# Performance work log

Hardware: AMD Instinct MI355X
Metric: run time of the kernel (lower is better)

The kernel has to match this reference:

```python
import jax, jax.numpy as jnp
import numpy as np

B, T, I = 16384, 101, 4
H = 512  # lstm_hidden_layer_size
M = 512  # mlp_hidden_layer_size


def setup_inputs() -> dict:
    key = jax.random.key(0)
    ks = jax.random.split(key, 10)
    s_ih = 1.0 / np.sqrt(H)
    inp = {
        "batch_x": jax.random.normal(ks[0], (B, T, I), dtype=jnp.float32),
        "batch_a": jax.random.uniform(ks[1], (B, 1), dtype=jnp.float32),
        # PyTorch nn.LSTM params (gate order i,f,g,o), U(-1/sqrt(H), 1/sqrt(H))
        "W_ih": jax.random.uniform(ks[2], (4 * H, I), minval=-s_ih, maxval=s_ih, dtype=jnp.float32),
        "W_hh": jax.random.uniform(ks[3], (4 * H, H), minval=-s_ih, maxval=s_ih, dtype=jnp.float32),
        "b_ih": jax.random.uniform(ks[4], (4 * H,), minval=-s_ih, maxval=s_ih, dtype=jnp.float32),
        "b_hh": jax.random.uniform(ks[5], (4 * H,), minval=-s_ih, maxval=s_ih, dtype=jnp.float32),
        "W1": jax.random.uniform(ks[6], (M, H), minval=-s_ih, maxval=s_ih, dtype=jnp.float32),
        "b1": jax.random.uniform(ks[7], (M,), minval=-s_ih, maxval=s_ih, dtype=jnp.float32),
        "W2": jax.random.uniform(ks[8], (1, M + 1), minval=-1.0 / np.sqrt(M + 1), maxval=1.0 / np.sqrt(M + 1), dtype=jnp.float32),
        "b2": jax.random.uniform(ks[9], (1,), minval=-1.0 / np.sqrt(M + 1), maxval=1.0 / np.sqrt(M + 1), dtype=jnp.float32),
    }
    return inp


def _lstm_last_hidden(batch_x, W_ih, W_hh, b_ih, b_hh):
    h = W_hh.shape[1]
    # input projections for all timesteps at once: [T, B, 4H]
    x_proj = jnp.einsum("bti,gi->tbg", batch_x, W_ih) + b_ih + b_hh

    def step(carry, xp):
        h_t, c_t = carry
        gates = xp + h_t @ W_hh.T  # [B, 4H]
        i, f, g, o = jnp.split(gates, 4, axis=-1)
        i = jax.nn.sigmoid(i)
        f = jax.nn.sigmoid(f)
        g = jnp.tanh(g)
        o = jax.nn.sigmoid(o)
        c_new = f * c_t + i * g
        h_new = o * jnp.tanh(c_new)
        return (h_new, c_new), None

    b = batch_x.shape[0]
    h0 = jnp.zeros((b, h), dtype=batch_x.dtype)
    c0 = jnp.zeros((b, h), dtype=batch_x.dtype)
    (h_T, _), _ = jax.lax.scan(step, (h0, c0), x_proj)
    return h_T  # [B, H]


def reference(batch_x, batch_a, W_ih, W_hh, b_ih, b_hh, W1, b1, W2, b2):
    h_T = _lstm_last_hidden(batch_x, W_ih, W_hh, b_ih, b_hh)
    x = jax.nn.relu(h_T @ W1.T + b1)
    # dropout(p=0.3) treated as identity (eval-mode) for a deterministic reference
    x = jnp.concatenate([x, batch_a], axis=1)  # [B, M+1]
    return x @ W2.T + b2  # [B, 1]
```

## Files before the change

kernel.cpp:

```cpp
#include <hip/hip_runtime.h>
#include <hip/hip_bf16.h>

#define BATCH 16384
#define TSTEPS 101
#define HDIM 512
#define GDIM 2048

typedef __attribute__((ext_vector_type(8))) short s16x8;
typedef __attribute__((ext_vector_type(4))) float f32x4;

__device__ __forceinline__ float sigm(float x){ return 1.0f/(1.0f + __expf(-x)); }
__device__ __forceinline__ float tanhx(float x){ float e=__expf(2.0f*x); return 1.0f - 2.0f/(e+1.0f); }

__device__ __forceinline__ void gload16(const void* g, void* l){
  __builtin_amdgcn_global_load_lds((const __attribute__((address_space(1))) unsigned int*)g,
                                   (__attribute__((address_space(3))) unsigned int*)l, 16, 0, 0);
}

__global__ __launch_bounds__(256, 2) void lstm_step(
    const __hip_bfloat16* __restrict__ hin,
    __hip_bfloat16* __restrict__ hout,
    float* __restrict__ cbuf,
    const float* __restrict__ bx,
    const float* __restrict__ Wih,
    const float* __restrict__ bcomb,
    const __hip_bfloat16* __restrict__ wbf,
    int t, int skipmm)
{
  __shared__ short sA[256*64];
  __shared__ short sB[128*64];
  const int tid = threadIdx.x;
  const int l = tid & 63, w = tid >> 6;
  const int lr = l & 15, lk = l >> 4;

  const int orig = blockIdx.x;
  const int swz = (orig & 7)*128 + (orig >> 3);
  const int m0 = (swz >> 4) * 256;
  const int j0 = (swz & 15) * 32;

  f32x4 acc[4][4][2] = {};

  if (!skipmm){
    for (int k0 = 0; k0 < HDIM; k0 += 64){
      __syncthreads();
      #pragma unroll
      for (int i = 0; i < 8; ++i){
        int cch = i*256 + tid;
        int row = cch >> 3, kc = cch & 7;
        int kcs = kc ^ (row & 7);
        gload16(hin + (size_t)(m0 + row)*HDIM + k0 + kcs*8, &sA[cch*8]);
      }
      #pragma unroll
      for (int i = 0; i < 4; ++i){
        int cch = i*256 + tid;
        int r = cch >> 3, kc = cch & 7;
        int kcs = kc ^ (r & 7);
        int wrow = (r >> 5)*HDIM + j0 + (r & 31);
        gload16(wbf + (size_t)wrow*HDIM + k0 + kcs*8, &sB[cch*8]);
      }
      __syncthreads();
      #pragma unroll
      for (int kk = 0; kk < 2; ++kk){
        s16x8 av[4];
        #pragma unroll
        for (int m = 0; m < 4; ++m){
          int row = w*64 + m*16 + lr;
          int slot = row*8 + ((kk*4 + lk) ^ (row & 7));
          av[m] = *(const s16x8*)&sA[slot*8];
        }
        #pragma unroll
        for (int g = 0; g < 4; ++g){
          #pragma unroll
          for (int n = 0; n < 2; ++n){
            int rB = g*32 + n*16 + lr;
            int slot = rB*8 + ((kk*4 + lk) ^ (rB & 7));
            s16x8 bv = *(const s16x8*)&sB[slot*8];
            #pragma unroll
            for (int m = 0; m < 4; ++m)
              acc[g][m][n] = __builtin_amdgcn_mfma_f32_16x16x32_bf16(av[m], bv, acc[g][m][n], 0, 0, 0);
          }
        }
      }
    }
  }

  float4 wv[4][2]; float bc[4][2];
  #pragma unroll
  for (int g = 0; g < 4; ++g){
    #pragma unroll
    for (int n = 0; n < 2; ++n){
      int col = j0 + n*16 + lr;
      int grow = g*HDIM + col;
      wv[g][n] = *(const float4*)(Wih + (size_t)grow*4);
      bc[g][n] = bcomb[grow];
    }
  }
  #pragma unroll
  for (int m = 0; m < 4; ++m){
    #pragma unroll
    for (int rg = 0; rg < 4; ++rg){
      int r = m0 + w*64 + m*16 + lk*4 + rg;
      float4 xv = *(const float4*)(bx + ((size_t)r*TSTEPS + t)*4);
      #pragma unroll
      for (int n = 0; n < 2; ++n){
        int col = j0 + n*16 + lr;
        float pi = acc[0][m][n][rg] + bc[0][n] + xv.x*wv[0][n].x + xv.y*wv[0][n].y + xv.z*wv[0][n].z + xv.w*wv[0][n].w;
        float pf = acc[1][m][n][rg] + bc[1][n] + xv.x*wv[1][n].x + xv.y*wv[1][n].y + xv.z*wv[1][n].z + xv.w*wv[1][n].w;
        float pg = acc[2][m][n][rg] + bc[2][n] + xv.x*wv[2][n].x + xv.y*wv[2][n].y + xv.z*wv[2][n].z + xv.w*wv[2][n].w;
        float po = acc[3][m][n][rg] + bc[3][n] + xv.x*wv[3][n].x + xv.y*wv[3][n].y + xv.z*wv[3][n].z + xv.w*wv[3][n].w;
        float iv = sigm(pi), fv = sigm(pf), gv = tanhx(pg), ov = sigm(po);
        size_t idx = (size_t)r*HDIM + col;
        float cn = fv*cbuf[idx] + iv*gv;
        cbuf[idx] = cn;
        hout[idx] = __float2bfloat16(ov*tanhx(cn));
      }
    }
  }
}

__global__ void prep(const float* __restrict__ Whh, const float* __restrict__ W1,
                     const float* __restrict__ bih, const float* __restrict__ bhh,
                     __hip_bfloat16* __restrict__ wbf, __hip_bfloat16* __restrict__ w1bf,
                     float* __restrict__ bcomb){
  int i = blockIdx.x*256 + threadIdx.x;
  if (i < GDIM*HDIM) wbf[i] = __float2bfloat16(Whh[i]);
  if (i < HDIM*HDIM) w1bf[i] = __float2bfloat16(W1[i]);
  if (i < GDIM) bcomb[i] = bih[i] + bhh[i];
}

__global__ __launch_bounds__(256) void mlp1(const __hip_bfloat16* __restrict__ hT,
                                            const __hip_bfloat16* __restrict__ w1bf,
                                            const float* __restrict__ b1, float* __restrict__ xout){
  __shared__ short sA[128*64];
  __shared__ short sB[128*64];
  const int tid = threadIdx.x;
  const int l = tid & 63, w = tid >> 6;
  const int lr = l & 15, lk = l >> 4;
  const int r0 = blockIdx.x * 128, c0 = blockIdx.y * 128;

  f32x4 acc[2][8] = {};
  for (int k0 = 0; k0 < HDIM; k0 += 64){
    __syncthreads();
    #pragma unroll
    for (int i = 0; i < 4; ++i){
      int cch = i*256 + tid;
      int row = cch >> 3, kc = cch & 7;
      int kcs = kc ^ (row & 7);
      gload16(hT + (size_t)(r0 + row)*HDIM + k0 + kcs*8, &sA[cch*8]);
    }
    #pragma unroll
    for (int i = 0; i < 4; ++i){
      int cch = i*256 + tid;
      int row = cch >> 3, kc = cch & 7;
      int kcs = kc ^ (row & 7);
      gload16(w1bf + (size_t)(c0 + row)*HDIM + k0 + kcs*8, &sB[cch*8]);
    }
    __syncthreads();
    #pragma unroll
    for (int kk = 0; kk < 2; ++kk){
      s16x8 av[2];
      #pragma unroll
      for (int m = 0; m < 2; ++m){
        int row = w*32 + m*16 + lr;
        int slot = row*8 + ((kk*4 + lk) ^ (row & 7));
        av[m] = *(const s16x8*)&sA[slot*8];
      }
      #pragma unroll
      for (int n = 0; n < 8; ++n){
        int rB = n*16 + lr;
        int slot = rB*8 + ((kk*4 + lk) ^ (rB & 7));
        s16x8 bv = *(const s16x8*)&sB[slot*8];
        #pragma unroll
        for (int m = 0; m < 2; ++m)
          acc[m][n] = __builtin_amdgcn_mfma_f32_16x16x32_bf16(av[m], bv, acc[m][n], 0, 0, 0);
      }
    }
  }
  #pragma unroll
  for (int m = 0; m < 2; ++m){
    #pragma unroll
    for (int rg = 0; rg < 4; ++rg){
      int r = r0 + w*32 + m*16 + lk*4 + rg;
      #pragma unroll
      for (int n = 0; n < 8; ++n){
        int c = c0 + n*16 + lr;
        float v = acc[m][n][rg] + b1[c];
        xout[(size_t)r*HDIM + c] = v > 0.f ? v : 0.f;
      }
    }
  }
}

__global__ __launch_bounds__(256) void mlp2(const float* __restrict__ x, const float* __restrict__ a,
                                            const float* __restrict__ W2, const float* __restrict__ b2,
                                            float* __restrict__ out){
  const int wi = threadIdx.x >> 6, l = threadIdx.x & 63;
  const int b = blockIdx.x*4 + wi;
  const float* xr = x + (size_t)b*HDIM;
  float4 v0 = *(const float4*)(xr + l*8);
  float4 v1 = *(const float4*)(xr + l*8 + 4);
  float4 w0 = *(const float4*)(W2 + l*8);
  float4 w1 = *(const float4*)(W2 + l*8 + 4);
  float s = v0.x*w0.x + v0.y*w0.y + v0.z*w0.z + v0.w*w0.w
          + v1.x*w1.x + v1.y*w1.y + v1.z*w1.z + v1.w*w1.w;
  #pragma unroll
  for (int off = 32; off > 0; off >>= 1) s += __shfl_down(s, off);
  if (l == 0) out[b] = s + a[b]*W2[HDIM] + b2[0];
}

extern "C" void kernel_launch(void* const* d_in, const int* in_sizes, int n_in,
                              void* d_out, int out_size, void* d_ws, size_t ws_size,
                              hipStream_t stream){
  const float* bx  = (const float*)d_in[0];
  const float* ba  = (const float*)d_in[1];
  const float* Wih = (const float*)d_in[2];
  const float* Whh = (const float*)d_in[3];
  const float* bih = (const float*)d_in[4];
  const float* bhh = (const float*)d_in[5];
  const float* W1  = (const float*)d_in[6];
  const float* b1  = (const float*)d_in[7];
  const float* W2  = (const float*)d_in[8];
  const float* b2  = (const float*)d_in[9];
  float* out = (float*)d_out;

  char* ws = (char*)d_ws;
  __hip_bfloat16* wbf   = (__hip_bfloat16*)(ws);
  __hip_bfloat16* w1bf  = (__hip_bfloat16*)(ws + 2097152);
  float*          bcomb = (float*)(ws + 2621440);
  __hip_bfloat16* hb0   = (__hip_bfloat16*)(ws + 2629632);
  __hip_bfloat16* hb1   = (__hip_bfloat16*)(ws + 19406848);
  float*          cbuf  = (float*)(ws + 36184064);
  float*          xmlp  = cbuf;

  prep<<<4096, 256, 0, stream>>>(Whh, W1, bih, bhh, wbf, w1bf, bcomb);
  hipMemsetAsync(cbuf, 0, (size_t)BATCH*HDIM*sizeof(float), stream);

  for (int t = 0; t < TSTEPS; ++t){
    const __hip_bfloat16* hin = (t & 1) ? hb1 : hb0;
    __hip_bfloat16*      hout = (t & 1) ? hb0 : hb1;
    lstm_step<<<1024, 256, 0, stream>>>(hin, hout, cbuf, bx, Wih, bcomb, wbf,
                                        t, (t == 0) ? 1 : 0);
  }
  mlp1<<<dim3(128, 4), 256, 0, stream>>>(hb1, w1bf, b1, xmlp);
  mlp2<<<4096, 256, 0, stream>>>(xmlp, ba, W2, b2, out);
}
```

Measured before the change: 5.676 ms.

## Double-buffer W_hh tiles in LDS and load h operand directly to registers

The per-step LSTM GEMM no longer stages the h tile through shared memory. Each wave now reads its A fragments straight from global memory into registers, and the weight tile is double-buffered in LDS so the next k-slice's loads are issued before the current slice's MFMAs run. This is meant to overlap global-load latency with compute and to remove half of the LDS traffic and one barrier per k-step. In exchange it uses more registers for the prefetched A fragments, which may hurt occupancy at launch_bounds(256,2), and the direct global A reads are less coalesced.

```diff
diff --git a/kernel.cpp b/kernel.cpp
--- a/kernel.cpp
+++ b/kernel.cpp
@@ -27,8 +27,7 @@
     const __hip_bfloat16* __restrict__ wbf,
     int t, int skipmm)
 {
-  __shared__ short sA[256*64];
-  __shared__ short sB[128*64];
+  __shared__ short sB[2][128*64];
   const int tid = threadIdx.x;
   const int l = tid & 63, w = tid >> 6;
   const int lr = l & 15, lk = l >> 4;
@@ -40,47 +39,77 @@
 
   f32x4 acc[4][4][2] = {};
 
+#define COMPUTE(AR, BUF)                                                        \
+  do {                                                                          \
+    _Pragma("unroll")                                                           \
+    for (int kk = 0; kk < 2; ++kk){                                             \
+      _Pragma("unroll")                                                         \
+      for (int g = 0; g < 4; ++g){                                              \
+        _Pragma("unroll")                                                       \
+        for (int n = 0; n < 2; ++n){                                            \
+          int rB = g*32 + n*16 + lr;                                            \
+          int slot = rB*8 + ((kk*4 + lk) ^ (rB & 7));                           \
+          s16x8 bv = *(const s16x8*)&sB[BUF][slot*8];                           \
+          _Pragma("unroll")                                                     \
+          for (int m = 0; m < 4; ++m)                                           \
+            acc[g][m][n] = __builtin_amdgcn_mfma_f32_16x16x32_bf16(AR[m*2+kk], bv, acc[g][m][n], 0, 0, 0); \
+        }                                                                       \
+      }                                                                         \
+    }                                                                           \
+  } while(0)
+
   if (!skipmm){
-    for (int k0 = 0; k0 < HDIM; k0 += 64){
+    int bch[4]; const __hip_bfloat16* bsrc[4];
+    #pragma unroll
+    for (int i = 0; i < 4; ++i){
+      int cch = i*256 + tid;
+      int r = cch >> 3, kc = cch & 7;
+      int kcs = kc ^ (r & 7);
+      bch[i] = cch*8;
+      bsrc[i] = wbf + (size_t)((r >> 5)*HDIM + j0 + (r & 31))*HDIM + kcs*8;
+    }
+    const __hip_bfloat16* arow[4];
+    #pragma unroll
+    for (int m = 0; m < 4; ++m)
+      arow[m] = hin + (size_t)(m0 + w*64 + m*16 + lr)*HDIM + lk*8;
+
+    s16x8 aE[8], aO[8];
+    #pragma unroll
+    for (int i = 0; i < 4; ++i) gload16(bsrc[i], &sB[0][bch[i]]);
+    #pragma unroll
+    for (int m = 0; m < 4; ++m){
+      aE[m*2+0] = *(const s16x8*)(arow[m]);
+      aE[m*2+1] = *(const s16x8*)(arow[m] + 32);
+    }
+    __syncthreads();
+
+    #pragma unroll
+    for (int kt2 = 0; kt2 < 4; ++kt2){
+      const int ko = kt2*2 + 1;
+      {
+        const int k0 = ko*64;
+        #pragma unroll
+        for (int i = 0; i < 4; ++i) gload16(bsrc[i] + k0, &sB[1][bch[i]]);
+        #pragma unroll
+        for (int m = 0; m < 4; ++m){
+          aO[m*2+0] = *(const s16x8*)(arow[m] + k0);
+          aO[m*2+1] = *(const s16x8*)(arow[m] + k0 + 32);
+        }
+      }
+      COMPUTE(aE, 0);
       __syncthreads();
-      #pragma unroll
-      for (int i = 0; i < 8; ++i){
-        int cch = i*256 + tid;
-        int row = cch >> 3, kc = cch & 7;
-        int kcs = kc ^ (row & 7);
-        gload16(hin + (size_t)(m0 + row)*HDIM + k0 + kcs*8, &sA[cch*8]);
-      }
-      #pragma unroll
-      for (int i = 0; i < 4; ++i){
-        int cch = i*256 + tid;
-        int r = cch >> 3, kc = cch & 7;
-        int kcs = kc ^ (r & 7);
-        int wrow = (r >> 5)*HDIM + j0 + (r & 31);
-        gload16(wbf + (size_t)wrow*HDIM + k0 + kcs*8, &sB[cch*8]);
-      }
+      if (ko < 7){
+        const int k0 = (ko+1)*64;
+        #pragma unroll
+        for (int i = 0; i < 4; ++i) gload16(bsrc[i] + k0, &sB[0][bch[i]]);
+        #pragma unroll
+        for (int m = 0; m < 4; ++m){
+          aE[m*2+0] = *(const s16x8*)(arow[m] + k0);
+          aE[m*2+1] = *(const s16x8*)(arow[m] + k0 + 32);
+        }
+      }
+      COMPUTE(aO, 1);
       __syncthreads();
-      #pragma unroll
-      for (int kk = 0; kk < 2; ++kk){
-        s16x8 av[4];
-        #pragma unroll
-        for (int m = 0; m < 4; ++m){
-          int row = w*64 + m*16 + lr;
-          int slot = row*8 + ((kk*4 + lk) ^ (row & 7));
-          av[m] = *(const s16x8*)&sA[slot*8];
-        }
-        #pragma unroll
-        for (int g = 0; g < 4; ++g){
-          #pragma unroll
-          for (int n = 0; n < 2; ++n){
-            int rB = g*32 + n*16 + lr;
-            int slot = rB*8 + ((kk*4 + lk) ^ (rB & 7));
-            s16x8 bv = *(const s16x8*)&sB[slot*8];
-            #pragma unroll
-            for (int m = 0; m < 4; ++m)
-              acc[g][m][n] = __builtin_amdgcn_mfma_f32_16x16x32_bf16(av[m], bv, acc[g][m][n], 0, 0, 0);
-          }
-        }
-      }
     }
   }
 
@@ -116,6 +145,7 @@
       }
     }
   }
+#undef COMPUTE
 }
 
 __global__ void prep(const float* __restrict__ Whh, const float* __restrict__ W1,
```

New measurement: 6.554 ms. 1.15x slower.

## Triple-buffer LDS tiles with async global-to-LDS prefetch in recurrent GEMM

Applied to the files above, without the earlier changes.

Replaces the single-buffered 64-wide K loop, which synchronized twice per tile, with a 3-stage ring of 32-wide K tiles. Loads are issued two stages ahead via global_load_lds and fenced with explicit vmcnt waits and one barrier per step. The LDS layout changes to a new rotation-based swizzle with precomputed per-thread source and destination addresses, and the MFMA section runs at raised wave priority. The aim is to overlap memory latency with MFMA work and cut barrier overhead. The cost is more LDS (72KB total), which may affect the 2-blocks-per-CU occupancy target.

```diff
diff --git a/kernel.cpp b/kernel.cpp
--- a/kernel.cpp
+++ b/kernel.cpp
@@ -27,8 +27,8 @@
     const __hip_bfloat16* __restrict__ wbf,
     int t, int skipmm)
 {
-  __shared__ short sA[256*64];
-  __shared__ short sB[128*64];
+  __shared__ short sA[3*8192];
+  __shared__ short sB[3*4096];
   const int tid = threadIdx.x;
   const int l = tid & 63, w = tid >> 6;
   const int lr = l & 15, lk = l >> 4;
@@ -41,47 +41,75 @@
   f32x4 acc[4][4][2] = {};
 
   if (!skipmm){
-    for (int k0 = 0; k0 < HDIM; k0 += 64){
-      __syncthreads();
-      #pragma unroll
-      for (int i = 0; i < 8; ++i){
-        int cch = i*256 + tid;
-        int row = cch >> 3, kc = cch & 7;
-        int kcs = kc ^ (row & 7);
-        gload16(hin + (size_t)(m0 + row)*HDIM + k0 + kcs*8, &sA[cch*8]);
-      }
-      #pragma unroll
-      for (int i = 0; i < 4; ++i){
-        int cch = i*256 + tid;
-        int r = cch >> 3, kc = cch & 7;
-        int kcs = kc ^ (r & 7);
-        int wrow = (r >> 5)*HDIM + j0 + (r & 31);
-        gload16(wbf + (size_t)wrow*HDIM + k0 + kcs*8, &sB[cch*8]);
-      }
-      __syncthreads();
-      #pragma unroll
-      for (int kk = 0; kk < 2; ++kk){
-        s16x8 av[4];
-        #pragma unroll
-        for (int m = 0; m < 4; ++m){
-          int row = w*64 + m*16 + lr;
-          int slot = row*8 + ((kk*4 + lk) ^ (row & 7));
-          av[m] = *(const s16x8*)&sA[slot*8];
-        }
-        #pragma unroll
-        for (int g = 0; g < 4; ++g){
-          #pragma unroll
-          for (int n = 0; n < 2; ++n){
-            int rB = g*32 + n*16 + lr;
-            int slot = rB*8 + ((kk*4 + lk) ^ (rB & 7));
-            s16x8 bv = *(const s16x8*)&sB[slot*8];
-            #pragma unroll
-            for (int m = 0; m < 4; ++m)
-              acc[g][m][n] = __builtin_amdgcn_mfma_f32_16x16x32_bf16(av[m], bv, acc[g][m][n], 0, 0, 0);
-          }
-        }
-      }
-    }
+    const __hip_bfloat16* asrc[4]; int adst[4];
+    #pragma unroll
+    for (int i = 0; i < 4; ++i){
+      int c = i*256 + tid;
+      int p = c >> 3, s = c & 7;
+      int row = p*2 + (s >> 2);
+      int lkg = ((s & 3) + 4 - (p & 3)) & 3;
+      asrc[i] = hin + (size_t)(m0 + row)*HDIM + lkg*8;
+      adst[i] = c*8;
+    }
+    const __hip_bfloat16* bsrc[2]; int bdst[2];
+    #pragma unroll
+    for (int i = 0; i < 2; ++i){
+      int c = i*256 + tid;
+      int p = c >> 3, s = c & 7;
+      int grow = p*2 + (s >> 2);
+      int lkg = ((s & 3) + 4 - (p & 3)) & 3;
+      int wrow = (grow >> 5)*HDIM + j0 + (grow & 31);
+      bsrc[i] = wbf + (size_t)wrow*HDIM + lkg*8;
+      bdst[i] = c*8;
+    }
+    const int raddA = (w*32 + (lr >> 1))*128 + ((lr & 1) << 6) + (((lk + (lr >> 1)) & 3) << 4);
+    const int raddB = ((lr >> 1))*128 + ((lr & 1) << 6) + (((lk + (lr >> 1)) & 3) << 4);
+    const short* pA = (const short*)((const char*)sA + raddA);
+    const short* pB = (const short*)((const char*)sB + raddB);
+
+#define STAGE(BI, KT) do{                                                        \
+    _Pragma("unroll")                                                            \
+    for (int i = 0; i < 2; ++i) gload16(bsrc[i] + (KT)*32, &sB[(BI)*4096 + bdst[i]]); \
+    _Pragma("unroll")                                                            \
+    for (int i = 0; i < 4; ++i) gload16(asrc[i] + (KT)*32, &sA[(BI)*8192 + adst[i]]); \
+  }while(0)
+
+#define COMPUTE(BI) do{                                                          \
+    s16x8 av[4];                                                                 \
+    _Pragma("unroll")                                                            \
+    for (int m = 0; m < 4; ++m) av[m] = *(const s16x8*)(pA + (BI)*8192 + m*512); \
+    __builtin_amdgcn_s_setprio(1);                                               \
+    _Pragma("unroll")                                                            \
+    for (int g = 0; g < 4; ++g){                                                 \
+      _Pragma("unroll")                                                          \
+      for (int n = 0; n < 2; ++n){                                               \
+        s16x8 bv = *(const s16x8*)(pB + (BI)*4096 + g*1024 + n*512);             \
+        _Pragma("unroll")                                                        \
+        for (int m = 0; m < 4; ++m)                                              \
+          acc[g][m][n] = __builtin_amdgcn_mfma_f32_16x16x32_bf16(av[m], bv, acc[g][m][n], 0, 0, 0); \
+      }                                                                          \
+    }                                                                            \
+    __builtin_amdgcn_s_setprio(0);                                               \
+  }while(0)
+
+    STAGE(0, 0);
+    STAGE(1, 1);
+    asm volatile("s_waitcnt vmcnt(6)" ::: "memory");
+    __builtin_amdgcn_s_barrier();
+    __builtin_amdgcn_sched_barrier(0);
+
+    #pragma unroll
+    for (int kt = 0; kt < 16; ++kt){
+      if (kt < 14) STAGE((kt + 2) % 3, kt + 2);
+      __builtin_amdgcn_sched_barrier(0);
+      COMPUTE(kt % 3);
+      if (kt <= 13) asm volatile("s_waitcnt vmcnt(6)" ::: "memory");
+      else          asm volatile("s_waitcnt vmcnt(0)" ::: "memory");
+      __builtin_amdgcn_s_barrier();
+      __builtin_amdgcn_sched_barrier(0);
+    }
+#undef STAGE
+#undef COMPUTE
   }
 
   float4 wv[4][2]; float bc[4][2];
```

Result: slower. 6.235 ms (+9.9%).

## Enlarge LSTM step tile to 256x256 with 32x32x16 MFMA and 512 threads

Applied to the files above, without the earlier changes.

The per-timestep recurrent GEMM now uses a 256-row by 64-hidden-column (256 gate columns) block tile with 8 waves instead of 256x32 with 4 waves. It switches from 16x16x32 to 32x32x16 bf16 MFMA and precomputes global-to-LDS load addresses. The aim is more reuse of the h tile across gates, since each h row is loaded by 8 column blocks instead of 16, and fewer LDS reads per MFMA. The cbuf memset is replaced by treating the old cell state as zero on the first step. The larger LDS footprint (64KB) and 512 threads per block may limit occupancy to one block per CU.

```diff
diff --git a/kernel.cpp b/kernel.cpp
--- a/kernel.cpp
+++ b/kernel.cpp
@@ -7,6 +7,7 @@
 #define GDIM 2048
 
 typedef __attribute__((ext_vector_type(8))) short s16x8;
+typedef __attribute__((ext_vector_type(16))) float f32x16;
 typedef __attribute__((ext_vector_type(4))) float f32x4;
 
 __device__ __forceinline__ float sigm(float x){ return 1.0f/(1.0f + __expf(-x)); }
@@ -17,7 +18,7 @@
                                    (__attribute__((address_space(3))) unsigned int*)l, 16, 0, 0);
 }
 
-__global__ __launch_bounds__(256, 2) void lstm_step(
+__global__ __launch_bounds__(512, 2) void lstm_step(
     const __hip_bfloat16* __restrict__ hin,
     __hip_bfloat16* __restrict__ hout,
     float* __restrict__ cbuf,
@@ -28,89 +29,84 @@
     int t, int skipmm)
 {
   __shared__ short sA[256*64];
-  __shared__ short sB[128*64];
+  __shared__ short sB[256*64];
   const int tid = threadIdx.x;
-  const int l = tid & 63, w = tid >> 6;
-  const int lr = l & 15, lk = l >> 4;
+  const int l  = tid & 63, w = tid >> 6;
+  const int lo = l & 31,  hi = l >> 5;
+  const int wr = w >> 1,  wc = w & 1;
 
   const int orig = blockIdx.x;
-  const int swz = (orig & 7)*128 + (orig >> 3);
-  const int m0 = (swz >> 4) * 256;
-  const int j0 = (swz & 15) * 32;
-
-  f32x4 acc[4][4][2] = {};
+  const int swz = (orig & 7)*64 + (orig >> 3);
+  const int panel = swz >> 3;
+  const int cq    = swz & 7;
+
+  f32x16 acc[4][2] = {};
 
   if (!skipmm){
-    for (int k0 = 0; k0 < HDIM; k0 += 64){
+    const __hip_bfloat16* asrc[4]; int adst[4];
+    const __hip_bfloat16* bsrc[4]; int bdst[4];
+    #pragma unroll
+    for (int i = 0; i < 4; ++i){
+      int c = i*512 + tid;
+      int row = c >> 3, s = c & 7;
+      int kc = s ^ (row & 7);
+      asrc[i] = hin + (size_t)(panel*256 + row)*HDIM + kc*8;
+      adst[i] = c*8;
+      int g = row >> 6, hcw = row & 63;
+      bsrc[i] = wbf + (size_t)(g*HDIM + cq*64 + hcw)*HDIM + kc*8;
+      bdst[i] = c*8;
+    }
+    const int xorv = (lo & 7);
+    const int rowA0 = wr*64 + lo, rowA1 = rowA0 + 32;
+
+    for (int kt = 0; kt < 8; ++kt){
+      const int k0 = kt*64;
       __syncthreads();
       #pragma unroll
-      for (int i = 0; i < 8; ++i){
-        int cch = i*256 + tid;
-        int row = cch >> 3, kc = cch & 7;
-        int kcs = kc ^ (row & 7);
-        gload16(hin + (size_t)(m0 + row)*HDIM + k0 + kcs*8, &sA[cch*8]);
-      }
-      #pragma unroll
-      for (int i = 0; i < 4; ++i){
-        int cch = i*256 + tid;
-        int r = cch >> 3, kc = cch & 7;
-        int kcs = kc ^ (r & 7);
-        int wrow = (r >> 5)*HDIM + j0 + (r & 31);
-        gload16(wbf + (size_t)wrow*HDIM + k0 + kcs*8, &sB[cch*8]);
-      }
+      for (int i = 0; i < 4; ++i) gload16(asrc[i] + k0, &sA[adst[i]]);
+      #pragma unroll
+      for (int i = 0; i < 4; ++i) gload16(bsrc[i] + k0, &sB[bdst[i]]);
       __syncthreads();
       #pragma unroll
-      for (int kk = 0; kk < 2; ++kk){
-        s16x8 av[4];
-        #pragma unroll
-        for (int m = 0; m < 4; ++m){
-          int row = w*64 + m*16 + lr;
-          int slot = row*8 + ((kk*4 + lk) ^ (row & 7));
-          av[m] = *(const s16x8*)&sA[slot*8];
-        }
+      for (int kk = 0; kk < 4; ++kk){
+        const int so = ((kk*2 + hi) ^ xorv) * 8;
+        s16x8 av0 = *(const s16x8*)&sA[rowA0*64 + so];
+        s16x8 av1 = *(const s16x8*)&sA[rowA1*64 + so];
         #pragma unroll
         for (int g = 0; g < 4; ++g){
-          #pragma unroll
-          for (int n = 0; n < 2; ++n){
-            int rB = g*32 + n*16 + lr;
-            int slot = rB*8 + ((kk*4 + lk) ^ (rB & 7));
-            s16x8 bv = *(const s16x8*)&sB[slot*8];
-            #pragma unroll
-            for (int m = 0; m < 4; ++m)
-              acc[g][m][n] = __builtin_amdgcn_mfma_f32_16x16x32_bf16(av[m], bv, acc[g][m][n], 0, 0, 0);
-          }
+          s16x8 bv = *(const s16x8*)&sB[(g*64 + wc*32 + lo)*64 + so];
+          acc[g][0] = __builtin_amdgcn_mfma_f32_32x32x16_bf16(av0, bv, acc[g][0], 0, 0, 0);
+          acc[g][1] = __builtin_amdgcn_mfma_f32_32x32x16_bf16(av1, bv, acc[g][1], 0, 0, 0);
         }
       }
     }
   }
 
-  float4 wv[4][2]; float bc[4][2];
+  const int colg = cq*64 + wc*32 + lo;
+  float4 wv[4]; float bc4[4];
   #pragma unroll
   for (int g = 0; g < 4; ++g){
-    #pragma unroll
-    for (int n = 0; n < 2; ++n){
-      int col = j0 + n*16 + lr;
-      int grow = g*HDIM + col;
-      wv[g][n] = *(const float4*)(Wih + (size_t)grow*4);
-      bc[g][n] = bcomb[grow];
-    }
-  }
-  #pragma unroll
-  for (int m = 0; m < 4; ++m){
-    #pragma unroll
-    for (int rg = 0; rg < 4; ++rg){
-      int r = m0 + w*64 + m*16 + lk*4 + rg;
-      float4 xv = *(const float4*)(bx + ((size_t)r*TSTEPS + t)*4);
-      #pragma unroll
-      for (int n = 0; n < 2; ++n){
-        int col = j0 + n*16 + lr;
-        float pi = acc[0][m][n][rg] + bc[0][n] + xv.x*wv[0][n].x + xv.y*wv[0][n].y + xv.z*wv[0][n].z + xv.w*wv[0][n].w;
-        float pf = acc[1][m][n][rg] + bc[1][n] + xv.x*wv[1][n].x + xv.y*wv[1][n].y + xv.z*wv[1][n].z + xv.w*wv[1][n].w;
-        float pg = acc[2][m][n][rg] + bc[2][n] + xv.x*wv[2][n].x + xv.y*wv[2][n].y + xv.z*wv[2][n].z + xv.w*wv[2][n].w;
-        float po = acc[3][m][n][rg] + bc[3][n] + xv.x*wv[3][n].x + xv.y*wv[3][n].y + xv.z*wv[3][n].z + xv.w*wv[3][n].w;
+    int gc = g*HDIM + colg;
+    wv[g]  = *(const float4*)(Wih + (size_t)gc*4);
+    bc4[g] = bcomb[gc];
+  }
+  #pragma unroll
+  for (int m = 0; m < 2; ++m){
+    #pragma unroll
+    for (int q = 0; q < 4; ++q){
+      #pragma unroll
+      for (int i2 = 0; i2 < 4; ++i2){
+        const int reg = q*4 + i2;
+        const int r = panel*256 + wr*64 + m*32 + q*8 + hi*4 + i2;
+        float4 xv = *(const float4*)(bx + ((size_t)r*TSTEPS + t)*4);
+        float pi = acc[0][m][reg] + bc4[0] + xv.x*wv[0].x + xv.y*wv[0].y + xv.z*wv[0].z + xv.w*wv[0].w;
+        float pf = acc[1][m][reg] + bc4[1] + xv.x*wv[1].x + xv.y*wv[1].y + xv.z*wv[1].z + xv.w*wv[1].w;
+        float pg = acc[2][m][reg] + bc4[2] + xv.x*wv[2].x + xv.y*wv[2].y + xv.z*wv[2].z + xv.w*wv[2].w;
+        float po = acc[3][m][reg] + bc4[3] + xv.x*wv[3].x + xv.y*wv[3].y + xv.z*wv[3].z + xv.w*wv[3].w;
         float iv = sigm(pi), fv = sigm(pf), gv = tanhx(pg), ov = sigm(po);
-        size_t idx = (size_t)r*HDIM + col;
-        float cn = fv*cbuf[idx] + iv*gv;
+        size_t idx = (size_t)r*HDIM + colg;
+        float cold = skipmm ? 0.f : cbuf[idx];
+        float cn = fv*cold + iv*gv;
         cbuf[idx] = cn;
         hout[idx] = __float2bfloat16(ov*tanhx(cn));
       }
@@ -233,13 +229,12 @@
   float*          xmlp  = cbuf;
 
   prep<<<4096, 256, 0, stream>>>(Whh, W1, bih, bhh, wbf, w1bf, bcomb);
-  hipMemsetAsync(cbuf, 0, (size_t)BATCH*HDIM*sizeof(float), stream);
 
   for (int t = 0; t < TSTEPS; ++t){
     const __hip_bfloat16* hin = (t & 1) ? hb1 : hb0;
     __hip_bfloat16*      hout = (t & 1) ? hb0 : hb1;
-    lstm_step<<<1024, 256, 0, stream>>>(hin, hout, cbuf, bx, Wih, bcomb, wbf,
-                                        t, (t == 0) ? 1 : 0);
+    lstm_step<<<512, 512, 0, stream>>>(hin, hout, cbuf, bx, Wih, bcomb, wbf,
+                                       t, (t == 0) ? 1 : 0);
   }
   mlp1<<<dim3(128, 4), 256, 0, stream>>>(hb1, w1bf, b1, xmlp);
   mlp2<<<4096, 256, 0, stream>>>(xmlp, ba, W2, b2, out);
```

New measurement: 7.040 ms. 24.0% more time.
